# Performance work log

Hardware: AMD Instinct MI355X
Metric: run time of the kernel (lower is better)

## Reference

```python
import jax, jax.numpy as jnp
import numpy as np

B, N, DIM = 32, 1024, 512
H, KD, ATTN_RATIO = 8, 64, 4
D = ATTN_RATIO * KD            # value dim per head = 256
DH = D * H                     # 2048
QKV_OUT = DH + 2 * H * KD      # 3072
RES = 32                       # resolution (32, 32), N = 32*32
SCALE = KD ** -0.5


def _make_bias_idxs(res):
    coords = np.stack(np.meshgrid(np.arange(res), np.arange(res), indexing="ij"), -1).reshape(-1, 2)  # [N,2]
    off = np.abs(coords[:, None, :] - coords[None, :, :])  # [N,N,2]
    return jnp.asarray(off[..., 0] * res + off[..., 1], dtype=jnp.int32)  # [N,N] in [0, res*res)


def setup_inputs() -> dict:
    key = jax.random.key(0)
    ks = jax.random.split(key, 6)
    x = jax.random.normal(ks[0], (B, N, DIM), dtype=jnp.float32)
    gamma = jnp.ones((DIM,), jnp.float32)
    beta = jnp.zeros((DIM,), jnp.float32)
    qkv_w = jax.random.normal(ks[1], (DIM, QKV_OUT), jnp.float32) * 0.02
    qkv_b = jnp.zeros((QKV_OUT,), jnp.float32)
    proj_w = jax.random.normal(ks[2], (DH, DIM), jnp.float32) * 0.02
    proj_b = jnp.zeros((DIM,), jnp.float32)
    biases = jax.random.normal(ks[3], (H, RES * RES), jnp.float32) * 0.02
    bias_idxs = _make_bias_idxs(RES)
    return {"x": x, "gamma": gamma, "beta": beta, "qkv_w": qkv_w, "qkv_b": qkv_b,
            "proj_w": proj_w, "proj_b": proj_b, "biases": biases, "bias_idxs": bias_idxs}


def reference(x, gamma, beta, qkv_w, qkv_b, proj_w, proj_b, biases, bias_idxs):
    # LayerNorm
    mu = jnp.mean(x, axis=-1, keepdims=True)
    var = jnp.mean(jnp.square(x - mu), axis=-1, keepdims=True)
    xn = (x - mu) * jax.lax.rsqrt(var + 1e-5) * gamma + beta
    # QKV projection and head split
    qkv = (xn @ qkv_w + qkv_b).reshape(B, N, H, 2 * KD + D)
    q, k, v = jnp.split(qkv, [KD, 2 * KD], axis=-1)  # [B,N,H,KD],[B,N,H,KD],[B,N,H,D]
    # Attention with relative-position bias
    bias = biases[:, bias_idxs]  # [H,N,N]
    attn = jnp.einsum("bqhd,bkhd->bhqk", q, k) * SCALE + bias[None]
    attn = jax.nn.softmax(attn, axis=-1)
    out = jnp.einsum("bhqk,bkhd->bqhd", attn, v).reshape(B, N, DH)
    return out @ proj_w + proj_b
```

## Files before the change

### kernel.cpp

```cpp
#include <hip/hip_runtime.h>
#include <hip/hip_bf16.h>
#include <initializer_list>

typedef _Float16 half8 __attribute__((ext_vector_type(8)));
typedef float floatx4 __attribute__((ext_vector_type(4)));

#define MFMA16(a, b, c) __builtin_amdgcn_mfma_f32_16x16x32_f16((a), (b), (c), 0, 0, 0)

__global__ __launch_bounds__(256) void ln_kernel(const float* __restrict__ x,
                                                 const float* __restrict__ gamma,
                                                 const float* __restrict__ beta,
                                                 _Float16* __restrict__ xn) {
    int row = blockIdx.x;
    int tid = threadIdx.x;
    float2 v = ((const float2*)(x + (size_t)row * 512))[tid];

    __shared__ float red[4];
    __shared__ float mv[2];

    float s = v.x + v.y;
#pragma unroll
    for (int o = 32; o > 0; o >>= 1) s += __shfl_down(s, o);
    if ((tid & 63) == 0) red[tid >> 6] = s;
    __syncthreads();
    if (tid == 0) mv[0] = (red[0] + red[1] + red[2] + red[3]) * (1.f / 512.f);
    __syncthreads();
    float mean = mv[0];

    float dx = v.x - mean, dy = v.y - mean;
    float sq = dx * dx + dy * dy;
#pragma unroll
    for (int o = 32; o > 0; o >>= 1) sq += __shfl_xor(sq, o);
    __syncthreads();
    if ((tid & 63) == 0) red[tid >> 6] = sq;
    __syncthreads();
    if (tid == 0) mv[1] = rsqrtf((red[0] + red[1] + red[2] + red[3]) * (1.f / 512.f) + 1e-5f);
    __syncthreads();
    float rstd = mv[1];

    float g0 = gamma[tid * 2], g1 = gamma[tid * 2 + 1];
    float b0 = beta[tid * 2], b1 = beta[tid * 2 + 1];
    union { _Float16 h[2]; unsigned int u; } pk;
    pk.h[0] = (_Float16)(dx * rstd * g0 + b0);
    pk.h[1] = (_Float16)(dy * rstd * g1 + b1);
    ((unsigned int*)(xn + (size_t)row * 512))[tid] = pk.u;
}

__global__ void transpose_cast(const float* __restrict__ in, _Float16* __restrict__ out,
                               int R, int C) {
    int idx = blockIdx.x * 256 + threadIdx.x;
    if (idx >= R * C) return;
    int orow = idx / R;
    int ocol = idx - orow * R;
    out[idx] = (_Float16)in[(size_t)ocol * C + orow];
}

template <int OUTMODE>
__global__ __launch_bounds__(256) void gemm_bt(const _Float16* __restrict__ A,
                                               const _Float16* __restrict__ Bt,
                                               const float* __restrict__ bias,
                                               void* __restrict__ Cout,
                                               _Float16* __restrict__ Vt,
                                               int M, int N, int K) {
    __shared__ __align__(16) _Float16 Asb[128 * 40];
    __shared__ __align__(16) _Float16 Bsb[128 * 40];

    int m0 = blockIdx.x * 128;
    int n0 = blockIdx.y * 128;
    int tid = threadIdx.x;
    int w = tid >> 6, lane = tid & 63, lrow = lane & 15, quad = lane >> 4;
    int wm = (w >> 1) * 64, wn = (w & 1) * 64;

    floatx4 acc[4][4];
#pragma unroll
    for (int i = 0; i < 4; ++i)
#pragma unroll
        for (int j = 0; j < 4; ++j) acc[i][j] = (floatx4){0.f, 0.f, 0.f, 0.f};

    for (int k0 = 0; k0 < K; k0 += 32) {
        __syncthreads();
#pragma unroll
        for (int it = 0; it < 2; ++it) {
            int c = tid + it * 256;
            int rr = c >> 2;
            int c8 = (c & 3) * 8;
            uint4 ta = *(const uint4*)(A + (size_t)(m0 + rr) * K + k0 + c8);
            uint4 tb = *(const uint4*)(Bt + (size_t)(n0 + rr) * K + k0 + c8);
            *(uint4*)&Asb[rr * 40 + c8] = ta;
            *(uint4*)&Bsb[rr * 40 + c8] = tb;
        }
        __syncthreads();

        half8 af[4], bf[4];
#pragma unroll
        for (int i = 0; i < 4; ++i)
            af[i] = *(const half8*)&Asb[(wm + i * 16 + lrow) * 40 + quad * 8];
#pragma unroll
        for (int j = 0; j < 4; ++j)
            bf[j] = *(const half8*)&Bsb[(wn + j * 16 + lrow) * 40 + quad * 8];
#pragma unroll
        for (int i = 0; i < 4; ++i)
#pragma unroll
            for (int j = 0; j < 4; ++j)
                acc[i][j] = MFMA16(af[i], bf[j], acc[i][j]);
    }

    int hh = blockIdx.y / 3;
    int part = blockIdx.y - hh * 3;

#pragma unroll
    for (int i = 0; i < 4; ++i)
#pragma unroll
        for (int j = 0; j < 4; ++j) {
            int colg = n0 + wn + j * 16 + lrow;
            int coll = wn + j * 16 + lrow;
            float bv = bias[colg];
#pragma unroll
            for (int r = 0; r < 4; ++r) {
                int rowg = m0 + wm + i * 16 + quad * 4 + r;
                float v = acc[i][j][r] + bv;
                if (OUTMODE == 1) {
                    ((float*)Cout)[(size_t)rowg * N + colg] = v;
                } else {
                    if (part == 0) {
                        ((_Float16*)Cout)[(size_t)rowg * 1024 + hh * 128 + coll] = (_Float16)v;
                    } else {
                        int d = (part - 1) * 128 + coll;
                        int b_rel = rowg >> 10;
                        int n = rowg & 1023;
                        Vt[(((size_t)b_rel * 8 + hh) * 256 + d) * 1024 + n] = (_Float16)v;
                    }
                }
            }
        }
}

__global__ __launch_bounds__(256) void attn_kernel(const _Float16* __restrict__ qk,
                                                   const _Float16* __restrict__ vt,
                                                   const float* __restrict__ biases,
                                                   _Float16* __restrict__ out) {
    int h  = blockIdx.x & 7;
    int qt = (blockIdx.x >> 3) | (blockIdx.y << 1);
    int b  = blockIdx.z;

    int tid = threadIdx.x;
    int w = tid >> 6, lane = tid & 63, lrow = lane & 15, quad = lane >> 4;

    __shared__ float bias_lds[1024];
    __shared__ __align__(16) _Float16 K_lds[32 * 72];
    __shared__ __align__(16) _Float16 V_t[256 * 32];

    for (int i = tid; i < 1024; i += 256) bias_lds[i] = biases[h * 1024 + i];

    int qrow = qt * 64 + w * 16 + lrow;
    const _Float16* qbase = qk + ((size_t)(b * 1024 + qrow)) * 1024 + h * 128;
    half8 aq0 = *(const half8*)(qbase + quad * 8);
    half8 aq1 = *(const half8*)(qbase + 32 + quad * 8);

    int key_l = tid >> 3, kd8 = (tid & 7) * 8;
    const _Float16* ksrc = qk + ((size_t)(b * 1024 + key_l)) * 1024 + h * 128 + 64 + kd8;
    int cc = tid & 3;
    const _Float16* vsrc0 = vt + ((size_t)((b * 8 + h) * 256 + (tid >> 2))) * 1024 + cc * 4;

    int qr = qrow >> 5, qc = qrow & 31;
    int bcol0[4], bcol1[4];
#pragma unroll
    for (int r = 0; r < 4; ++r) {
        bcol0[r] = abs(qc - (quad * 4 + r));
        bcol1[r] = abs(qc - (16 + quad * 4 + r));
    }

    float m_r = -1e30f, l_r = 0.f;
    floatx4 od[16];
#pragma unroll
    for (int dt = 0; dt < 16; ++dt) od[dt] = (floatx4){0.f, 0.f, 0.f, 0.f};

    uint4 kreg;
    uint2 vA[4], vB[4];

    kreg = *(const uint4*)ksrc;
#pragma unroll
    for (int it = 0; it < 4; ++it) {
        const _Float16* p = vsrc0 + (size_t)it * 64 * 1024;
        vA[it] = *(const uint2*)p;
        vB[it] = *(const uint2*)(p + 16);
    }

    for (int kt = 0; kt < 32; ++kt) {
        *(uint4*)&K_lds[key_l * 72 + kd8] = kreg;
#pragma unroll
        for (int it = 0; it < 4; ++it) {
            uint4 v;
            v.x = vA[it].x; v.y = vA[it].y; v.z = vB[it].x; v.w = vB[it].y;
            *(uint4*)&V_t[((tid >> 2) + it * 64) * 32 + cc * 8] = v;
        }
        __syncthreads();

        if (kt < 31) {
            kreg = *(const uint4*)(ksrc + (size_t)(kt + 1) * 32 * 1024);
            const _Float16* vp = vsrc0 + (size_t)(kt + 1) * 32;
#pragma unroll
            for (int it = 0; it < 4; ++it) {
                const _Float16* p = vp + (size_t)it * 64 * 1024;
                vA[it] = *(const uint2*)p;
                vB[it] = *(const uint2*)(p + 16);
            }
        }

        floatx4 sc0 = (floatx4){0.f, 0.f, 0.f, 0.f}, sc1 = sc0;
        {
            half8 kf;
            kf = *(const half8*)&K_lds[lrow * 72 + quad * 8];              sc0 = MFMA16(kf, aq0, sc0);
            kf = *(const half8*)&K_lds[lrow * 72 + 32 + quad * 8];         sc0 = MFMA16(kf, aq1, sc0);
            kf = *(const half8*)&K_lds[(16 + lrow) * 72 + quad * 8];       sc1 = MFMA16(kf, aq0, sc1);
            kf = *(const half8*)&K_lds[(16 + lrow) * 72 + 32 + quad * 8];  sc1 = MFMA16(kf, aq1, sc1);
        }

        int rowoff = abs(qr - kt) << 5;
        float s0[4], s1[4];
#pragma unroll
        for (int r = 0; r < 4; ++r) {
            s0[r] = sc0[r] * 0.125f + bias_lds[rowoff + bcol0[r]];
            s1[r] = sc1[r] * 0.125f + bias_lds[rowoff + bcol1[r]];
        }

        float pmax = fmaxf(fmaxf(fmaxf(s0[0], s0[1]), fmaxf(s0[2], s0[3])),
                           fmaxf(fmaxf(s1[0], s1[1]), fmaxf(s1[2], s1[3])));
        pmax = fmaxf(pmax, __shfl_xor(pmax, 16));
        pmax = fmaxf(pmax, __shfl_xor(pmax, 32));

        if (!__all(pmax - m_r <= 8.f)) {
            float mnew = fmaxf(m_r, pmax);
            float alpha = __expf(m_r - mnew);
            m_r = mnew;
            l_r *= alpha;
            float a4[4];
#pragma unroll
            for (int r = 0; r < 4; ++r) a4[r] = __shfl(alpha, quad * 4 + r, 16);
#pragma unroll
            for (int dt = 0; dt < 16; ++dt)
#pragma unroll
                for (int r = 0; r < 4; ++r) od[dt][r] *= a4[r];
        }

        float p0[4], p1[4], rs = 0.f;
#pragma unroll
        for (int r = 0; r < 4; ++r) { p0[r] = __expf(s0[r] - m_r); rs += p0[r]; }
#pragma unroll
        for (int r = 0; r < 4; ++r) { p1[r] = __expf(s1[r] - m_r); rs += p1[r]; }
        rs += __shfl_xor(rs, 16);
        rs += __shfl_xor(rs, 32);
        l_r += rs;

        union H8 { _Float16 h[8]; half8 v; } pa;
#pragma unroll
        for (int r = 0; r < 4; ++r) { pa.h[r] = (_Float16)p0[r]; pa.h[4 + r] = (_Float16)p1[r]; }

#pragma unroll
        for (int dt = 0; dt < 16; ++dt) {
            half8 bv = *(const half8*)&V_t[(dt * 16 + lrow) * 32 + quad * 8];
            od[dt] = MFMA16(pa.v, bv, od[dt]);
        }
        __syncthreads();
    }

#pragma unroll
    for (int r = 0; r < 4; ++r) {
        float lq = __shfl(l_r, quad * 4 + r, 16);
        float inv = 1.f / lq;
        int qg = qt * 64 + w * 16 + quad * 4 + r;
        _Float16* orow = out + ((size_t)(b * 1024 + qg)) * 2048 + h * 256;
#pragma unroll
        for (int dt = 0; dt < 16; ++dt)
            orow[dt * 16 + lrow] = (_Float16)(od[dt][r] * inv);
    }
}

extern "C" void kernel_launch(void* const* d_in, const int* in_sizes, int n_in,
                              void* d_out, int out_size, void* d_ws, size_t ws_size,
                              hipStream_t stream) {
    const float* x      = (const float*)d_in[0];
    const float* gamma  = (const float*)d_in[1];
    const float* beta   = (const float*)d_in[2];
    const float* qkv_w  = (const float*)d_in[3];
    const float* qkv_b  = (const float*)d_in[4];
    const float* proj_w = (const float*)d_in[5];
    const float* proj_b = (const float*)d_in[6];
    const float* biases = (const float*)d_in[7];

    float* out = (float*)d_out;

    _Float16* ws      = (_Float16*)d_ws;
    _Float16* qkv_wt  = ws;
    _Float16* proj_wt = qkv_wt + (size_t)512 * 3072;
    _Float16* xn      = proj_wt + (size_t)2048 * 512;
    _Float16* chunk0  = xn + (size_t)32768 * 512;

    const size_t FIXED_HALVES = (size_t)512 * 3072 + (size_t)2048 * 512 + (size_t)32768 * 512;
    int CB = 0;
    for (int cb : {16, 8, 4, 2, 1}) {
        size_t halves = FIXED_HALVES + (size_t)cb * 1024 * (1024 + 2048 + 2048);
        if (halves * sizeof(_Float16) <= ws_size) { CB = cb; break; }
    }
    if (CB == 0) return;
    _Float16* qk_c  = chunk0;
    _Float16* vt_c  = qk_c + (size_t)CB * 1024 * 1024;
    _Float16* att_c = vt_c + (size_t)CB * 1024 * 2048;

    transpose_cast<<<(512 * 3072 + 255) / 256, 256, 0, stream>>>(qkv_w, qkv_wt, 512, 3072);
    transpose_cast<<<(2048 * 512 + 255) / 256, 256, 0, stream>>>(proj_w, proj_wt, 2048, 512);
    ln_kernel<<<32768, 256, 0, stream>>>(x, gamma, beta, xn);

    const int MC = CB * 1024;
    for (int c = 0; c < 32 / CB; ++c) {
        const _Float16* xn_c = xn + (size_t)c * MC * 512;
        gemm_bt<2><<<dim3(MC / 128, 24), 256, 0, stream>>>(xn_c, qkv_wt, qkv_b,
                                                           (void*)qk_c, vt_c, MC, 3072, 512);
        attn_kernel<<<dim3(16, 8, CB), 256, 0, stream>>>(qk_c, vt_c, biases, att_c);
        float* out_c = out + (size_t)c * MC * 512;
        gemm_bt<1><<<dim3(MC / 128, 4), 256, 0, stream>>>(att_c, proj_wt, proj_b,
                                                          (void*)out_c, nullptr, MC, 512, 2048);
    }
}
```

Baseline: 857.0 us.

## Use direct global-to-LDS loads in GEMM, tile transposes, pad V tile, exp2 softmax

The GEMM now loads A and B tiles with global_load_lds straight into unpadded LDS, using an XOR swizzle in place of the padding to avoid bank conflicts, so the data no longer passes through registers. The weight transpose-cast becomes a 32x32 tiled LDS transpose, giving coalesced reads and writes. In attention, the V tile gets padded rows, the bias and scale fold in log2(e) so the softmax can use exp2f, and the probabilities are packed to fp16 with cvt_pkrtz. These are several independent changes; round-toward-zero packing slightly alters numerics.

```diff
diff --git a/kernel.cpp b/kernel.cpp
--- a/kernel.cpp
+++ b/kernel.cpp
@@ -6,6 +6,12 @@
 typedef float floatx4 __attribute__((ext_vector_type(4)));
 
 #define MFMA16(a, b, c) __builtin_amdgcn_mfma_f32_16x16x32_f16((a), (b), (c), 0, 0, 0)
+
+__device__ __forceinline__ void gload16(const void* g, void* l) {
+    __builtin_amdgcn_global_load_lds((const __attribute__((address_space(1))) unsigned int*)g,
+                                     (__attribute__((address_space(3))) unsigned int*)l,
+                                     16, 0, 0);
+}
 
 __global__ __launch_bounds__(256) void ln_kernel(const float* __restrict__ x,
                                                  const float* __restrict__ gamma,
@@ -46,13 +52,19 @@
     ((unsigned int*)(xn + (size_t)row * 512))[tid] = pk.u;
 }
 
-__global__ void transpose_cast(const float* __restrict__ in, _Float16* __restrict__ out,
-                               int R, int C) {
-    int idx = blockIdx.x * 256 + threadIdx.x;
-    if (idx >= R * C) return;
-    int orow = idx / R;
-    int ocol = idx - orow * R;
-    out[idx] = (_Float16)in[(size_t)ocol * C + orow];
+__global__ __launch_bounds__(256) void transpose_cast(const float* __restrict__ in,
+                                                      _Float16* __restrict__ out,
+                                                      int R, int C) {
+    __shared__ float t[32][33];
+    int c0 = blockIdx.x * 32, r0 = blockIdx.y * 32;
+    int tx = threadIdx.x & 31, ty = threadIdx.x >> 5;
+#pragma unroll
+    for (int j = 0; j < 4; ++j)
+        t[ty + j * 8][tx] = in[(size_t)(r0 + ty + j * 8) * C + c0 + tx];
+    __syncthreads();
+#pragma unroll
+    for (int j = 0; j < 4; ++j)
+        out[(size_t)(c0 + ty + j * 8) * R + r0 + tx] = (_Float16)t[tx][ty + j * 8];
 }
 
 template <int OUTMODE>
@@ -62,8 +74,8 @@
                                                void* __restrict__ Cout,
                                                _Float16* __restrict__ Vt,
                                                int M, int N, int K) {
-    __shared__ __align__(16) _Float16 Asb[128 * 40];
-    __shared__ __align__(16) _Float16 Bsb[128 * 40];
+    __shared__ __align__(16) _Float16 Asb[128 * 32];
+    __shared__ __align__(16) _Float16 Bsb[128 * 32];
 
     int m0 = blockIdx.x * 128;
     int n0 = blockIdx.y * 128;
@@ -71,6 +83,16 @@
     int w = tid >> 6, lane = tid & 63, lrow = lane & 15, quad = lane >> 4;
     int wm = (w >> 1) * 64, wn = (w & 1) * 64;
 
+    int srow = lane >> 2;
+    int scb = (lane & 3) ^ ((lane >> 3) & 3);
+    const _Float16* Abase = A + (size_t)(m0 + w * 16 + srow) * K + scb * 8;
+    const _Float16* Bbase = Bt + (size_t)(n0 + w * 16 + srow) * K + scb * 8;
+    char* AldsB = (char*)Asb + w * 1024;
+    char* BldsB = (char*)Bsb + w * 1024;
+    const size_t rowskip = (size_t)64 * K;
+
+    int swz = (lrow >> 1) & 3;
+
     floatx4 acc[4][4];
 #pragma unroll
     for (int i = 0; i < 4; ++i)
@@ -79,25 +101,23 @@
 
     for (int k0 = 0; k0 < K; k0 += 32) {
         __syncthreads();
-#pragma unroll
-        for (int it = 0; it < 2; ++it) {
-            int c = tid + it * 256;
-            int rr = c >> 2;
-            int c8 = (c & 3) * 8;
-            uint4 ta = *(const uint4*)(A + (size_t)(m0 + rr) * K + k0 + c8);
-            uint4 tb = *(const uint4*)(Bt + (size_t)(n0 + rr) * K + k0 + c8);
-            *(uint4*)&Asb[rr * 40 + c8] = ta;
-            *(uint4*)&Bsb[rr * 40 + c8] = tb;
-        }
+        gload16(Abase + k0, AldsB);
+        gload16(Abase + rowskip + k0, AldsB + 4096);
+        gload16(Bbase + k0, BldsB);
+        gload16(Bbase + rowskip + k0, BldsB + 4096);
         __syncthreads();
 
         half8 af[4], bf[4];
 #pragma unroll
-        for (int i = 0; i < 4; ++i)
-            af[i] = *(const half8*)&Asb[(wm + i * 16 + lrow) * 40 + quad * 8];
-#pragma unroll
-        for (int j = 0; j < 4; ++j)
-            bf[j] = *(const half8*)&Bsb[(wn + j * 16 + lrow) * 40 + quad * 8];
+        for (int i = 0; i < 4; ++i) {
+            int r = wm + i * 16 + lrow;
+            af[i] = *(const half8*)&Asb[r * 32 + (quad ^ swz) * 8];
+        }
+#pragma unroll
+        for (int j = 0; j < 4; ++j) {
+            int r = wn + j * 16 + lrow;
+            bf[j] = *(const half8*)&Bsb[r * 32 + (quad ^ swz) * 8];
+        }
 #pragma unroll
         for (int i = 0; i < 4; ++i)
 #pragma unroll
@@ -148,9 +168,10 @@
 
     __shared__ float bias_lds[1024];
     __shared__ __align__(16) _Float16 K_lds[32 * 72];
-    __shared__ __align__(16) _Float16 V_t[256 * 32];
-
-    for (int i = tid; i < 1024; i += 256) bias_lds[i] = biases[h * 1024 + i];
+    __shared__ __align__(16) _Float16 V_t[256 * 40];
+
+    const float LOG2E = 1.44269504f;
+    for (int i = tid; i < 1024; i += 256) bias_lds[i] = biases[h * 1024 + i] * LOG2E;
 
     int qrow = qt * 64 + w * 16 + lrow;
     const _Float16* qbase = qk + ((size_t)(b * 1024 + qrow)) * 1024 + h * 128;
@@ -186,13 +207,15 @@
         vB[it] = *(const uint2*)(p + 16);
     }
 
+    const float SCL = 0.125f * LOG2E;
+
     for (int kt = 0; kt < 32; ++kt) {
         *(uint4*)&K_lds[key_l * 72 + kd8] = kreg;
 #pragma unroll
         for (int it = 0; it < 4; ++it) {
             uint4 v;
             v.x = vA[it].x; v.y = vA[it].y; v.z = vB[it].x; v.w = vB[it].y;
-            *(uint4*)&V_t[((tid >> 2) + it * 64) * 32 + cc * 8] = v;
+            *(uint4*)&V_t[((tid >> 2) + it * 64) * 40 + cc * 8] = v;
         }
         __syncthreads();
 
@@ -220,8 +243,8 @@
         float s0[4], s1[4];
 #pragma unroll
         for (int r = 0; r < 4; ++r) {
-            s0[r] = sc0[r] * 0.125f + bias_lds[rowoff + bcol0[r]];
-            s1[r] = sc1[r] * 0.125f + bias_lds[rowoff + bcol1[r]];
+            s0[r] = sc0[r] * SCL + bias_lds[rowoff + bcol0[r]];
+            s1[r] = sc1[r] * SCL + bias_lds[rowoff + bcol1[r]];
         }
 
         float pmax = fmaxf(fmaxf(fmaxf(s0[0], s0[1]), fmaxf(s0[2], s0[3])),
@@ -231,7 +254,7 @@
 
         if (!__all(pmax - m_r <= 8.f)) {
             float mnew = fmaxf(m_r, pmax);
-            float alpha = __expf(m_r - mnew);
+            float alpha = exp2f(m_r - mnew);
             m_r = mnew;
             l_r *= alpha;
             float a4[4];
@@ -245,20 +268,22 @@
 
         float p0[4], p1[4], rs = 0.f;
 #pragma unroll
-        for (int r = 0; r < 4; ++r) { p0[r] = __expf(s0[r] - m_r); rs += p0[r]; }
-#pragma unroll
-        for (int r = 0; r < 4; ++r) { p1[r] = __expf(s1[r] - m_r); rs += p1[r]; }
+        for (int r = 0; r < 4; ++r) { p0[r] = exp2f(s0[r] - m_r); rs += p0[r]; }
+#pragma unroll
+        for (int r = 0; r < 4; ++r) { p1[r] = exp2f(s1[r] - m_r); rs += p1[r]; }
         rs += __shfl_xor(rs, 16);
         rs += __shfl_xor(rs, 32);
         l_r += rs;
 
-        union H8 { _Float16 h[8]; half8 v; } pa;
-#pragma unroll
-        for (int r = 0; r < 4; ++r) { pa.h[r] = (_Float16)p0[r]; pa.h[4 + r] = (_Float16)p1[r]; }
+        union { unsigned int u[4]; half8 v; } pa;
+        pa.u[0] = __builtin_bit_cast(unsigned int, __builtin_amdgcn_cvt_pkrtz(p0[0], p0[1]));
+        pa.u[1] = __builtin_bit_cast(unsigned int, __builtin_amdgcn_cvt_pkrtz(p0[2], p0[3]));
+        pa.u[2] = __builtin_bit_cast(unsigned int, __builtin_amdgcn_cvt_pkrtz(p1[0], p1[1]));
+        pa.u[3] = __builtin_bit_cast(unsigned int, __builtin_amdgcn_cvt_pkrtz(p1[2], p1[3]));
 
 #pragma unroll
         for (int dt = 0; dt < 16; ++dt) {
-            half8 bv = *(const half8*)&V_t[(dt * 16 + lrow) * 32 + quad * 8];
+            half8 bv = *(const half8*)&V_t[(dt * 16 + lrow) * 40 + quad * 8];
             od[dt] = MFMA16(pa.v, bv, od[dt]);
         }
         __syncthreads();
@@ -307,8 +332,8 @@
     _Float16* vt_c  = qk_c + (size_t)CB * 1024 * 1024;
     _Float16* att_c = vt_c + (size_t)CB * 1024 * 2048;
 
-    transpose_cast<<<(512 * 3072 + 255) / 256, 256, 0, stream>>>(qkv_w, qkv_wt, 512, 3072);
-    transpose_cast<<<(2048 * 512 + 255) / 256, 256, 0, stream>>>(proj_w, proj_wt, 2048, 512);
+    transpose_cast<<<dim3(3072 / 32, 512 / 32), 256, 0, stream>>>(qkv_w, qkv_wt, 512, 3072);
+    transpose_cast<<<dim3(512 / 32, 2048 / 32), 256, 0, stream>>>(proj_w, proj_wt, 2048, 512);
     ln_kernel<<<32768, 256, 0, stream>>>(x, gamma, beta, xn);
 
     const int MC = CB * 1024;
```

After: 859.0 us. Within noise of the previous version (+0.2%).
